# Kernel tuning notes

Hardware: AMD Instinct MI355X
Metric: run time of the kernel (lower is better)

The kernel has to match this reference:

```python
import jax, jax.numpy as jnp
import numpy as np

B, C, H, W = 16, 256, 64, 64
NH, HD = 8, 32  # num_heads, head_dim


def _conv1x1(x, w, b):
    # x: [B,C,H,W], w: [Cout,Cin], b: [Cout] -> [B,Cout,H,W]
    return jnp.einsum('bchw,oc->bohw', x, w) + b[None, :, None, None]


def setup_inputs() -> dict:
    key = jax.random.key(0)
    ks = jax.random.split(key, 11)
    s = 1.0 / np.sqrt(C)
    return {
        'q': jax.random.normal(ks[0], (B, C, H, W), jnp.float32),
        'k': jax.random.normal(ks[1], (B, C, H, W), jnp.float32),
        'v': jax.random.normal(ks[2], (B, C, H, W), jnp.float32),
        'Wq': jax.random.normal(ks[3], (C, C), jnp.float32) * s,
        'bq': jax.random.normal(ks[4], (C,), jnp.float32) * 0.01,
        'Wk': jax.random.normal(ks[5], (C, C), jnp.float32) * s,
        'bk': jax.random.normal(ks[6], (C,), jnp.float32) * 0.01,
        'Wv': jax.random.normal(ks[7], (C, C), jnp.float32) * s,
        'bv': jax.random.normal(ks[8], (C,), jnp.float32) * 0.01,
        'Wo': jax.random.normal(ks[9], (C, C), jnp.float32) * s,
        'bo': jax.random.normal(ks[10], (C,), jnp.float32) * 0.01,
    }


def reference(q, k, v, Wq, bq, Wk, bk, Wv, bv, Wo, bo):
    # 1x1 conv projections, then split heads: [B, NH, HD, H, W]
    qh = _conv1x1(q, Wq, bq).reshape(B, NH, HD, H, W)
    kh = _conv1x1(k, Wk, bk).reshape(B, NH, HD, H, W)
    vh = _conv1x1(v, Wv, bv).reshape(B, NH, HD, H, W)
    # Attention over last two dims: q @ k^T -> [B, NH, HD, H, H], d_k = W
    scale = 1.0 / jnp.sqrt(jnp.float32(W))
    logits = jnp.einsum('bndhw,bndgw->bndhg', qh, kh) * scale
    attn = jax.nn.softmax(logits, axis=-1)  # [B,NH,HD,H,H]
    out = jnp.einsum('bndhg,bndgw->bndhw', attn, vh)  # [B,NH,HD,H,W]
    out = out.reshape(B, C, H, W)  # combine heads
    out = _conv1x1(out, Wo, bo)
    return out, attn
```

## Files before the change

### kernel.cpp

```cpp
#include <hip/hip_runtime.h>

#define NB  16
#define CC  256
#define SH  64
#define SW  64
#define HWP 4096
#define NSLICE (NB * CC)
#define OUT_ELEMS ((size_t)NB * CC * HWP)
#define PADK 40

using bf16x8 = __attribute__((ext_vector_type(8))) short;
using f32x4  = __attribute__((ext_vector_type(4))) float;

__device__ __forceinline__ unsigned pack_hi16(unsigned u0, unsigned u1) {
    return __builtin_amdgcn_perm(u1, u0, 0x07060302u);
}
__device__ __forceinline__ float trunc_bf(unsigned u) {
    union { unsigned u; float f; } v; v.u = u & 0xFFFF0000u; return v.f;
}
__device__ __forceinline__ unsigned fbits(float x) {
    union { float f; unsigned u; } v; v.f = x; return v.u;
}

__global__ __launch_bounds__(256) void proj_mfma_kernel(
    const float* __restrict__ X, const float* __restrict__ W,
    const float* __restrict__ bias, float* __restrict__ Y)
{
    __shared__ short sWhi[128][PADK];
    __shared__ short sWlo[128][PADK];
    __shared__ short sXhi[128][PADK];
    __shared__ short sXlo[128][PADK];

    const int tid = threadIdx.x;
    const int o0  = blockIdx.x * 128;
    const int p0  = blockIdx.y * 128;
    const int b   = blockIdx.z;
    const float* Xb = X + (size_t)b * CC * HWP;

    const int wid  = tid >> 6;
    const int lane = tid & 63;
    const int wr = wid >> 1, wc = wid & 1;
    const int l16 = lane & 15, lq = lane >> 4;

    const int kq = tid & 7;
    const int ooB = tid >> 3;
    const int cb = tid & 7;
    const int pb = tid >> 3;

    f32x4 acc[4][4] = {};

    for (int c0 = 0; c0 < CC; c0 += 32) {
        __syncthreads();

        #pragma unroll
        for (int pass = 0; pass < 4; ++pass) {
            const int oo = ooB + pass * 32;
            const float4 wv = *(const float4*)&W[(size_t)(o0 + oo) * CC + c0 + kq * 4];
            const unsigned u0 = fbits(wv.x), u1 = fbits(wv.y),
                           u2 = fbits(wv.z), u3 = fbits(wv.w);
            const float r0 = wv.x - trunc_bf(u0);
            const float r1 = wv.y - trunc_bf(u1);
            const float r2 = wv.z - trunc_bf(u2);
            const float r3 = wv.w - trunc_bf(u3);
            uint2 hi, lo;
            hi.x = pack_hi16(u0, u1);          hi.y = pack_hi16(u2, u3);
            lo.x = pack_hi16(fbits(r0), fbits(r1));
            lo.y = pack_hi16(fbits(r2), fbits(r3));
            *(uint2*)&sWhi[oo][kq * 4] = hi;
            *(uint2*)&sWlo[oo][kq * 4] = lo;
        }

        {
            const float* xsrc = Xb + (size_t)(c0 + cb * 4) * HWP + p0 + pb * 4;
            const float4 x0 = *(const float4*)(xsrc);
            const float4 x1 = *(const float4*)(xsrc + HWP);
            const float4 x2 = *(const float4*)(xsrc + 2 * HWP);
            const float4 x3 = *(const float4*)(xsrc + 3 * HWP);
            const float c0v[4][4] = {{x0.x, x1.x, x2.x, x3.x},
                                     {x0.y, x1.y, x2.y, x3.y},
                                     {x0.z, x1.z, x2.z, x3.z},
                                     {x0.w, x1.w, x2.w, x3.w}};
            #pragma unroll
            for (int j = 0; j < 4; ++j) {
                const unsigned u0 = fbits(c0v[j][0]), u1 = fbits(c0v[j][1]),
                               u2 = fbits(c0v[j][2]), u3 = fbits(c0v[j][3]);
                const float r0 = c0v[j][0] - trunc_bf(u0);
                const float r1 = c0v[j][1] - trunc_bf(u1);
                const float r2 = c0v[j][2] - trunc_bf(u2);
                const float r3 = c0v[j][3] - trunc_bf(u3);
                uint2 hi, lo;
                hi.x = pack_hi16(u0, u1);          hi.y = pack_hi16(u2, u3);
                lo.x = pack_hi16(fbits(r0), fbits(r1));
                lo.y = pack_hi16(fbits(r2), fbits(r3));
                *(uint2*)&sXhi[pb * 4 + j][cb * 4] = hi;
                *(uint2*)&sXlo[pb * 4 + j][cb * 4] = lo;
            }
        }
        __syncthreads();

        const int aRow = wr * 64 + l16;
        const int bRow = wc * 64 + l16;
        bf16x8 bhi[4], blo[4];
        #pragma unroll
        for (int fn = 0; fn < 4; ++fn) {
            bhi[fn] = *(const bf16x8*)&sXhi[bRow + fn * 16][lq * 8];
            blo[fn] = *(const bf16x8*)&sXlo[bRow + fn * 16][lq * 8];
        }
        #pragma unroll
        for (int fm = 0; fm < 4; ++fm) {
            const bf16x8 ahi = *(const bf16x8*)&sWhi[aRow + fm * 16][lq * 8];
            const bf16x8 alo = *(const bf16x8*)&sWlo[aRow + fm * 16][lq * 8];
            #pragma unroll
            for (int fn = 0; fn < 4; ++fn) {
                acc[fm][fn] = __builtin_amdgcn_mfma_f32_16x16x32_bf16(
                    ahi, bhi[fn], acc[fm][fn], 0, 0, 0);
                acc[fm][fn] = __builtin_amdgcn_mfma_f32_16x16x32_bf16(
                    ahi, blo[fn], acc[fm][fn], 0, 0, 0);
                acc[fm][fn] = __builtin_amdgcn_mfma_f32_16x16x32_bf16(
                    alo, bhi[fn], acc[fm][fn], 0, 0, 0);
            }
        }
    }

    #pragma unroll
    for (int fm = 0; fm < 4; ++fm) {
        #pragma unroll
        for (int j = 0; j < 4; ++j) {
            const int o = o0 + wr * 64 + fm * 16 + lq * 4 + j;
            const float bv = bias[o];
            #pragma unroll
            for (int fn = 0; fn < 4; ++fn) {
                Y[((size_t)b * CC + o) * HWP + p0 + wc * 64 + fn * 16 + l16] =
                    acc[fm][fn][j] + bv;
            }
        }
    }
}

__global__ __launch_bounds__(256) void attn_kernel(
    const float* qh, const float* kh, const float* vh,
    float* attn_out, float* out_pre)
{
    __shared__ float Qt[64][68];
    __shared__ float Kt[64][68];
    __shared__ float Vs[64][68];

    const int tid  = threadIdx.x;
    const int tr   = tid & 15;
    const int tc   = tid >> 4;
    const int s    = blockIdx.x;
    const size_t base = (size_t)s * HWP;

    {
        const int r0 = tc << 2, c0 = tr << 2;
        const float* src = qh + base + r0 * SW + c0;
        const float4 a0 = *(const float4*)(src);
        const float4 a1 = *(const float4*)(src + SW);
        const float4 a2 = *(const float4*)(src + 2 * SW);
        const float4 a3 = *(const float4*)(src + 3 * SW);
        *(float4*)&Qt[c0 + 0][r0] = make_float4(a0.x, a1.x, a2.x, a3.x);
        *(float4*)&Qt[c0 + 1][r0] = make_float4(a0.y, a1.y, a2.y, a3.y);
        *(float4*)&Qt[c0 + 2][r0] = make_float4(a0.z, a1.z, a2.z, a3.z);
        *(float4*)&Qt[c0 + 3][r0] = make_float4(a0.w, a1.w, a2.w, a3.w);
    }
    {
        const int r0 = tc << 2, c0 = tr << 2;
        const float* src = kh + base + r0 * SW + c0;
        const float4 a0 = *(const float4*)(src);
        const float4 a1 = *(const float4*)(src + SW);
        const float4 a2 = *(const float4*)(src + 2 * SW);
        const float4 a3 = *(const float4*)(src + 3 * SW);
        *(float4*)&Kt[c0 + 0][r0] = make_float4(a0.x, a1.x, a2.x, a3.x);
        *(float4*)&Kt[c0 + 1][r0] = make_float4(a0.y, a1.y, a2.y, a3.y);
        *(float4*)&Kt[c0 + 2][r0] = make_float4(a0.z, a1.z, a2.z, a3.z);
        *(float4*)&Kt[c0 + 3][r0] = make_float4(a0.w, a1.w, a2.w, a3.w);
    }
    #pragma unroll
    for (int it = 0; it < 4; ++it) {
        const int g = tc + it * 16;
        const float4 vv = *(const float4*)&vh[base + g * SW + (tr << 2)];
        *(float4*)&Vs[g][tr << 2] = vv;
    }
    __syncthreads();

    float accq[4][4] = {};
    #pragma unroll
    for (int w = 0; w < 64; ++w) {
        const float4 av = *(const float4*)&Qt[w][tc << 2];
        const float4 bv = *(const float4*)&Kt[w][tr << 2];
        const float a[4] = {av.x, av.y, av.z, av.w};
        const float g[4] = {bv.x, bv.y, bv.z, bv.w};
        #pragma unroll
        for (int i = 0; i < 4; ++i)
            #pragma unroll
            for (int j = 0; j < 4; ++j)
                accq[i][j] = fmaf(a[i], g[j], accq[i][j]);
    }

    float p[4][4];
    #pragma unroll
    for (int i = 0; i < 4; ++i) {
        float l0 = accq[i][0] * 0.125f;
        float l1 = accq[i][1] * 0.125f;
        float l2 = accq[i][2] * 0.125f;
        float l3 = accq[i][3] * 0.125f;
        float m = fmaxf(fmaxf(l0, l1), fmaxf(l2, l3));
        m = fmaxf(m, __shfl_xor(m, 1));
        m = fmaxf(m, __shfl_xor(m, 2));
        m = fmaxf(m, __shfl_xor(m, 4));
        m = fmaxf(m, __shfl_xor(m, 8));
        const float e0 = __expf(l0 - m);
        const float e1 = __expf(l1 - m);
        const float e2 = __expf(l2 - m);
        const float e3 = __expf(l3 - m);
        float sum = e0 + e1 + e2 + e3;
        sum += __shfl_xor(sum, 1);
        sum += __shfl_xor(sum, 2);
        sum += __shfl_xor(sum, 4);
        sum += __shfl_xor(sum, 8);
        const float rs = 1.0f / sum;
        p[i][0] = e0 * rs; p[i][1] = e1 * rs;
        p[i][2] = e2 * rs; p[i][3] = e3 * rs;
    }

    #pragma unroll
    for (int i = 0; i < 4; ++i) {
        float4 r = make_float4(p[i][0], p[i][1], p[i][2], p[i][3]);
        *(float4*)&attn_out[base + (size_t)((tc << 2) + i) * SH + (tr << 2)] = r;
    }

    __syncthreads();
    #pragma unroll
    for (int j = 0; j < 4; ++j) {
        *(float4*)&Qt[(tr << 2) + j][tc << 2] =
            make_float4(p[0][j], p[1][j], p[2][j], p[3][j]);
    }
    __syncthreads();

    float o[4][4] = {};
    #pragma unroll
    for (int g = 0; g < 64; ++g) {
        const float4 av = *(const float4*)&Qt[g][tc << 2];
        const float4 bv = *(const float4*)&Vs[g][tr << 2];
        const float a[4] = {av.x, av.y, av.z, av.w};
        const float v[4] = {bv.x, bv.y, bv.z, bv.w};
        #pragma unroll
        for (int i = 0; i < 4; ++i)
            #pragma unroll
            for (int j = 0; j < 4; ++j)
                o[i][j] = fmaf(a[i], v[j], o[i][j]);
    }
    #pragma unroll
    for (int i = 0; i < 4; ++i) {
        float4 r = make_float4(o[i][0], o[i][1], o[i][2], o[i][3]);
        *(float4*)&out_pre[base + (size_t)((tc << 2) + i) * SW + (tr << 2)] = r;
    }
}

extern "C" void kernel_launch(void* const* d_in, const int* in_sizes, int n_in,
                              void* d_out, int out_size, void* d_ws, size_t ws_size,
                              hipStream_t stream) {
    (void)in_sizes; (void)n_in; (void)out_size; (void)ws_size;

    const float* q  = (const float*)d_in[0];
    const float* k  = (const float*)d_in[1];
    const float* v  = (const float*)d_in[2];
    const float* Wq = (const float*)d_in[3];
    const float* bq = (const float*)d_in[4];
    const float* Wk = (const float*)d_in[5];
    const float* bk = (const float*)d_in[6];
    const float* Wv = (const float*)d_in[7];
    const float* bv = (const float*)d_in[8];
    const float* Wo = (const float*)d_in[9];
    const float* bo = (const float*)d_in[10];

    float* out  = (float*)d_out;
    float* attn = out + OUT_ELEMS;

    float* vh      = out;
    float* kh      = attn;
    float* qh      = (float*)d_ws;
    float* out_pre = qh;

    const dim3 gproj(2, 32, NB);
    const dim3 blk(256);

    proj_mfma_kernel<<<gproj, blk, 0, stream>>>(q, Wq, bq, qh);
    proj_mfma_kernel<<<gproj, blk, 0, stream>>>(k, Wk, bk, kh);
    proj_mfma_kernel<<<gproj, blk, 0, stream>>>(v, Wv, bv, vh);

    attn_kernel<<<dim3(NSLICE), blk, 0, stream>>>(qh, kh, vh, attn, out_pre);

    proj_mfma_kernel<<<gproj, blk, 0, stream>>>(out_pre, Wo, bo, out);
}
```

Before: 463.3 us.

## Use split-bf16 MFMA for attention and merge QKV projections into one launch

Rewrites the per-slice attention kernel so each wavefront handles one 64x64 slice. Both matmuls (QK^T and PV) run on bf16 MFMA with a hi/lo three-product split to keep near-fp32 accuracy, replacing scalar fp32 FMAs and the block-wide LDS transposes. The three Q/K/V projections become one launch with a 48-deep z grid to cut launch overhead and improve GPU fill. The costs are strided global loads for V, narrower attn/out stores, and more register pressure from holding K and V fragments.

```diff
diff --git a/kernel.cpp b/kernel.cpp
--- a/kernel.cpp
+++ b/kernel.cpp
@@ -12,19 +12,35 @@
 using bf16x8 = __attribute__((ext_vector_type(8))) short;
 using f32x4  = __attribute__((ext_vector_type(4))) float;
 
-__device__ __forceinline__ unsigned pack_hi16(unsigned u0, unsigned u1) {
+static __device__ __forceinline__ unsigned pack_hi16(unsigned u0, unsigned u1) {
     return __builtin_amdgcn_perm(u1, u0, 0x07060302u);
 }
-__device__ __forceinline__ float trunc_bf(unsigned u) {
+static __device__ __forceinline__ float trunc_bf(unsigned u) {
     union { unsigned u; float f; } v; v.u = u & 0xFFFF0000u; return v.f;
 }
-__device__ __forceinline__ unsigned fbits(float x) {
+static __device__ __forceinline__ unsigned fbits(float x) {
     union { float f; unsigned u; } v; v.f = x; return v.u;
 }
 
-__global__ __launch_bounds__(256) void proj_mfma_kernel(
+static __device__ __forceinline__ void split8(float4 a, float4 b,
+                                              bf16x8& hi, bf16x8& lo) {
+    union { bf16x8 v; unsigned u[4]; } H, L;
+    const float f[8] = {a.x, a.y, a.z, a.w, b.x, b.y, b.z, b.w};
+    #pragma unroll
+    for (int j = 0; j < 4; ++j) {
+        const unsigned u0 = fbits(f[2 * j]), u1 = fbits(f[2 * j + 1]);
+        const float r0 = f[2 * j]     - trunc_bf(u0);
+        const float r1 = f[2 * j + 1] - trunc_bf(u1);
+        H.u[j] = pack_hi16(u0, u1);
+        L.u[j] = pack_hi16(fbits(r0), fbits(r1));
+    }
+    hi = H.v; lo = L.v;
+}
+
+static __device__ __forceinline__ void proj_body(
     const float* __restrict__ X, const float* __restrict__ W,
-    const float* __restrict__ bias, float* __restrict__ Y)
+    const float* __restrict__ bias, float* __restrict__ Y,
+    int b, int o0, int p0)
 {
     __shared__ short sWhi[128][PADK];
     __shared__ short sWlo[128][PADK];
@@ -32,9 +48,6 @@
     __shared__ short sXlo[128][PADK];
 
     const int tid = threadIdx.x;
-    const int o0  = blockIdx.x * 128;
-    const int p0  = blockIdx.y * 128;
-    const int b   = blockIdx.z;
     const float* Xb = X + (size_t)b * CC * HWP;
 
     const int wid  = tid >> 6;
@@ -51,7 +64,6 @@
 
     for (int c0 = 0; c0 < CC; c0 += 32) {
         __syncthreads();
-
         #pragma unroll
         for (int pass = 0; pass < 4; ++pass) {
             const int oo = ooB + pass * 32;
@@ -69,7 +81,6 @@
             *(uint2*)&sWhi[oo][kq * 4] = hi;
             *(uint2*)&sWlo[oo][kq * 4] = lo;
         }
-
         {
             const float* xsrc = Xb + (size_t)(c0 + cb * 4) * HWP + p0 + pb * 4;
             const float4 x0 = *(const float4*)(xsrc);
@@ -137,123 +148,155 @@
     }
 }
 
-__global__ __launch_bounds__(256) void attn_kernel(
+__global__ __launch_bounds__(256) void proj_qkv_kernel(
+    const float* __restrict__ q, const float* __restrict__ Wq,
+    const float* __restrict__ bq, float* __restrict__ qh,
+    const float* __restrict__ k, const float* __restrict__ Wk,
+    const float* __restrict__ bk, float* __restrict__ kh,
+    const float* __restrict__ v, const float* __restrict__ Wv,
+    const float* __restrict__ bv, float* __restrict__ vh)
+{
+    const int which = blockIdx.z >> 4;
+    const int b     = blockIdx.z & 15;
+    const float* X  = (which == 0) ? q  : (which == 1) ? k  : v;
+    const float* W  = (which == 0) ? Wq : (which == 1) ? Wk : Wv;
+    const float* bi = (which == 0) ? bq : (which == 1) ? bk : bv;
+    float*       Y  = (which == 0) ? qh : (which == 1) ? kh : vh;
+    proj_body(X, W, bi, Y, b, blockIdx.x * 128, blockIdx.y * 128);
+}
+
+__global__ __launch_bounds__(256) void proj_o_kernel(
+    const float* __restrict__ X, const float* __restrict__ W,
+    const float* __restrict__ bias, float* __restrict__ Y)
+{
+    proj_body(X, W, bias, Y, blockIdx.z, blockIdx.x * 128, blockIdx.y * 128);
+}
+
+__global__ __launch_bounds__(256) void attn_mfma_kernel(
     const float* qh, const float* kh, const float* vh,
     float* attn_out, float* out_pre)
 {
-    __shared__ float Qt[64][68];
-    __shared__ float Kt[64][68];
-    __shared__ float Vs[64][68];
+    __shared__ float Pb[4][16][68];
 
     const int tid  = threadIdx.x;
-    const int tr   = tid & 15;
-    const int tc   = tid >> 4;
-    const int s    = blockIdx.x;
+    const int wid  = tid >> 6;
+    const int lane = tid & 63;
+    const int l16  = lane & 15;
+    const int lq   = lane >> 4;
+
+    const int s = blockIdx.x * 4 + wid;
     const size_t base = (size_t)s * HWP;
-
-    {
-        const int r0 = tc << 2, c0 = tr << 2;
-        const float* src = qh + base + r0 * SW + c0;
-        const float4 a0 = *(const float4*)(src);
-        const float4 a1 = *(const float4*)(src + SW);
-        const float4 a2 = *(const float4*)(src + 2 * SW);
-        const float4 a3 = *(const float4*)(src + 3 * SW);
-        *(float4*)&Qt[c0 + 0][r0] = make_float4(a0.x, a1.x, a2.x, a3.x);
-        *(float4*)&Qt[c0 + 1][r0] = make_float4(a0.y, a1.y, a2.y, a3.y);
-        *(float4*)&Qt[c0 + 2][r0] = make_float4(a0.z, a1.z, a2.z, a3.z);
-        *(float4*)&Qt[c0 + 3][r0] = make_float4(a0.w, a1.w, a2.w, a3.w);
-    }
-    {
-        const int r0 = tc << 2, c0 = tr << 2;
-        const float* src = kh + base + r0 * SW + c0;
-        const float4 a0 = *(const float4*)(src);
-        const float4 a1 = *(const float4*)(src + SW);
-        const float4 a2 = *(const float4*)(src + 2 * SW);
-        const float4 a3 = *(const float4*)(src + 3 * SW);
-        *(float4*)&Kt[c0 + 0][r0] = make_float4(a0.x, a1.x, a2.x, a3.x);
-        *(float4*)&Kt[c0 + 1][r0] = make_float4(a0.y, a1.y, a2.y, a3.y);
-        *(float4*)&Kt[c0 + 2][r0] = make_float4(a0.z, a1.z, a2.z, a3.z);
-        *(float4*)&Kt[c0 + 3][r0] = make_float4(a0.w, a1.w, a2.w, a3.w);
-    }
-    #pragma unroll
-    for (int it = 0; it < 4; ++it) {
-        const int g = tc + it * 16;
-        const float4 vv = *(const float4*)&vh[base + g * SW + (tr << 2)];
-        *(float4*)&Vs[g][tr << 2] = vv;
-    }
-    __syncthreads();
-
-    float accq[4][4] = {};
-    #pragma unroll
-    for (int w = 0; w < 64; ++w) {
-        const float4 av = *(const float4*)&Qt[w][tc << 2];
-        const float4 bv = *(const float4*)&Kt[w][tr << 2];
-        const float a[4] = {av.x, av.y, av.z, av.w};
-        const float g[4] = {bv.x, bv.y, bv.z, bv.w};
-        #pragma unroll
-        for (int i = 0; i < 4; ++i)
-            #pragma unroll
-            for (int j = 0; j < 4; ++j)
-                accq[i][j] = fmaf(a[i], g[j], accq[i][j]);
-    }
-
-    float p[4][4];
-    #pragma unroll
-    for (int i = 0; i < 4; ++i) {
-        float l0 = accq[i][0] * 0.125f;
-        float l1 = accq[i][1] * 0.125f;
-        float l2 = accq[i][2] * 0.125f;
-        float l3 = accq[i][3] * 0.125f;
-        float m = fmaxf(fmaxf(l0, l1), fmaxf(l2, l3));
-        m = fmaxf(m, __shfl_xor(m, 1));
-        m = fmaxf(m, __shfl_xor(m, 2));
-        m = fmaxf(m, __shfl_xor(m, 4));
-        m = fmaxf(m, __shfl_xor(m, 8));
-        const float e0 = __expf(l0 - m);
-        const float e1 = __expf(l1 - m);
-        const float e2 = __expf(l2 - m);
-        const float e3 = __expf(l3 - m);
-        float sum = e0 + e1 + e2 + e3;
-        sum += __shfl_xor(sum, 1);
-        sum += __shfl_xor(sum, 2);
-        sum += __shfl_xor(sum, 4);
-        sum += __shfl_xor(sum, 8);
-        const float rs = 1.0f / sum;
-        p[i][0] = e0 * rs; p[i][1] = e1 * rs;
-        p[i][2] = e2 * rs; p[i][3] = e3 * rs;
-    }
-
-    #pragma unroll
-    for (int i = 0; i < 4; ++i) {
-        float4 r = make_float4(p[i][0], p[i][1], p[i][2], p[i][3]);
-        *(float4*)&attn_out[base + (size_t)((tc << 2) + i) * SH + (tr << 2)] = r;
-    }
-
-    __syncthreads();
-    #pragma unroll
-    for (int j = 0; j < 4; ++j) {
-        *(float4*)&Qt[(tr << 2) + j][tc << 2] =
-            make_float4(p[0][j], p[1][j], p[2][j], p[3][j]);
-    }
-    __syncthreads();
-
-    float o[4][4] = {};
-    #pragma unroll
-    for (int g = 0; g < 64; ++g) {
-        const float4 av = *(const float4*)&Qt[g][tc << 2];
-        const float4 bv = *(const float4*)&Vs[g][tr << 2];
-        const float a[4] = {av.x, av.y, av.z, av.w};
-        const float v[4] = {bv.x, bv.y, bv.z, bv.w};
-        #pragma unroll
-        for (int i = 0; i < 4; ++i)
-            #pragma unroll
-            for (int j = 0; j < 4; ++j)
-                o[i][j] = fmaf(a[i], v[j], o[i][j]);
-    }
-    #pragma unroll
-    for (int i = 0; i < 4; ++i) {
-        float4 r = make_float4(o[i][0], o[i][1], o[i][2], o[i][3]);
-        *(float4*)&out_pre[base + (size_t)((tc << 2) + i) * SW + (tr << 2)] = r;
+    const float* Q = qh + base;
+    const float* K = kh + base;
+    const float* V = vh + base;
+    float (*P)[68] = Pb[wid];
+
+    bf16x8 Khi[4][2], Klo[4][2];
+    #pragma unroll
+    for (int nt = 0; nt < 4; ++nt)
+        #pragma unroll
+        for (int ks = 0; ks < 2; ++ks) {
+            const float* src = K + (nt * 16 + l16) * SW + ks * 32 + lq * 8;
+            split8(*(const float4*)src, *(const float4*)(src + 4),
+                   Khi[nt][ks], Klo[nt][ks]);
+        }
+
+    f32x4 acc[4][4] = {};
+    #pragma unroll
+    for (int mt = 0; mt < 4; ++mt) {
+        bf16x8 Qhi[2], Qlo[2];
+        #pragma unroll
+        for (int ks = 0; ks < 2; ++ks) {
+            const float* src = Q + (mt * 16 + l16) * SW + ks * 32 + lq * 8;
+            split8(*(const float4*)src, *(const float4*)(src + 4),
+                   Qhi[ks], Qlo[ks]);
+        }
+        #pragma unroll
+        for (int nt = 0; nt < 4; ++nt)
+            #pragma unroll
+            for (int ks = 0; ks < 2; ++ks) {
+                acc[mt][nt] = __builtin_amdgcn_mfma_f32_16x16x32_bf16(
+                    Qhi[ks], Khi[nt][ks], acc[mt][nt], 0, 0, 0);
+                acc[mt][nt] = __builtin_amdgcn_mfma_f32_16x16x32_bf16(
+                    Qhi[ks], Klo[nt][ks], acc[mt][nt], 0, 0, 0);
+                acc[mt][nt] = __builtin_amdgcn_mfma_f32_16x16x32_bf16(
+                    Qlo[ks], Khi[nt][ks], acc[mt][nt], 0, 0, 0);
+            }
+    }
+
+    bf16x8 Vhi[4][2], Vlo[4][2];
+    #pragma unroll
+    for (int nt = 0; nt < 4; ++nt)
+        #pragma unroll
+        for (int ks = 0; ks < 2; ++ks) {
+            const float* vcol = V + nt * 16 + l16;
+            float f[8];
+            #pragma unroll
+            for (int e = 0; e < 8; ++e)
+                f[e] = vcol[(ks * 32 + lq * 8 + e) * SW];
+            split8(make_float4(f[0], f[1], f[2], f[3]),
+                   make_float4(f[4], f[5], f[6], f[7]),
+                   Vhi[nt][ks], Vlo[nt][ks]);
+        }
+
+    #pragma unroll
+    for (int mt = 0; mt < 4; ++mt) {
+        #pragma unroll
+        for (int r = 0; r < 4; ++r) {
+            float l0 = acc[mt][0][r] * 0.125f;
+            float l1 = acc[mt][1][r] * 0.125f;
+            float l2 = acc[mt][2][r] * 0.125f;
+            float l3 = acc[mt][3][r] * 0.125f;
+            float m = fmaxf(fmaxf(l0, l1), fmaxf(l2, l3));
+            m = fmaxf(m, __shfl_xor(m, 1));
+            m = fmaxf(m, __shfl_xor(m, 2));
+            m = fmaxf(m, __shfl_xor(m, 4));
+            m = fmaxf(m, __shfl_xor(m, 8));
+            const float e0 = __expf(l0 - m);
+            const float e1 = __expf(l1 - m);
+            const float e2 = __expf(l2 - m);
+            const float e3 = __expf(l3 - m);
+            float sum = e0 + e1 + e2 + e3;
+            sum += __shfl_xor(sum, 1);
+            sum += __shfl_xor(sum, 2);
+            sum += __shfl_xor(sum, 4);
+            sum += __shfl_xor(sum, 8);
+            const float rs = 1.0f / sum;
+            const float p0 = e0 * rs, p1 = e1 * rs, p2 = e2 * rs, p3 = e3 * rs;
+            const int h = mt * 16 + lq * 4 + r;
+            float* gdst = attn_out + base + (size_t)h * SH;
+            gdst[0 * 16 + l16] = p0;
+            gdst[1 * 16 + l16] = p1;
+            gdst[2 * 16 + l16] = p2;
+            gdst[3 * 16 + l16] = p3;
+            const int hr = lq * 4 + r;
+            P[hr][0 * 16 + l16] = p0;
+            P[hr][1 * 16 + l16] = p1;
+            P[hr][2 * 16 + l16] = p2;
+            P[hr][3 * 16 + l16] = p3;
+        }
+        f32x4 o[4] = {};
+        #pragma unroll
+        for (int ks = 0; ks < 2; ++ks) {
+            const float* src = &P[l16][ks * 32 + lq * 8];
+            bf16x8 Phi, Plo;
+            split8(*(const float4*)src, *(const float4*)(src + 4), Phi, Plo);
+            #pragma unroll
+            for (int nt = 0; nt < 4; ++nt) {
+                o[nt] = __builtin_amdgcn_mfma_f32_16x16x32_bf16(
+                    Phi, Vhi[nt][ks], o[nt], 0, 0, 0);
+                o[nt] = __builtin_amdgcn_mfma_f32_16x16x32_bf16(
+                    Phi, Vlo[nt][ks], o[nt], 0, 0, 0);
+                o[nt] = __builtin_amdgcn_mfma_f32_16x16x32_bf16(
+                    Plo, Vhi[nt][ks], o[nt], 0, 0, 0);
+            }
+        }
+        #pragma unroll
+        for (int nt = 0; nt < 4; ++nt)
+            #pragma unroll
+            for (int r = 0; r < 4; ++r)
+                out_pre[base + (size_t)(mt * 16 + lq * 4 + r) * SW + nt * 16 + l16] =
+                    o[nt][r];
     }
 }
 
@@ -282,14 +325,13 @@
     float* qh      = (float*)d_ws;
     float* out_pre = qh;
 
-    const dim3 gproj(2, 32, NB);
     const dim3 blk(256);
 
-    proj_mfma_kernel<<<gproj, blk, 0, stream>>>(q, Wq, bq, qh);
-    proj_mfma_kernel<<<gproj, blk, 0, stream>>>(k, Wk, bk, kh);
-    proj_mfma_kernel<<<gproj, blk, 0, stream>>>(v, Wv, bv, vh);
-
-    attn_kernel<<<dim3(NSLICE), blk, 0, stream>>>(qh, kh, vh, attn, out_pre);
-
-    proj_mfma_kernel<<<gproj, blk, 0, stream>>>(out_pre, Wo, bo, out);
-}
+    proj_qkv_kernel<<<dim3(2, 32, 48), blk, 0, stream>>>(
+        q, Wq, bq, qh, k, Wk, bk, kh, v, Wv, bv, vh);
+
+    attn_mfma_kernel<<<dim3(NSLICE / 4), blk, 0, stream>>>(
+        qh, kh, vh, attn, out_pre);
+
+    proj_o_kernel<<<dim3(2, 32, 16), blk, 0, stream>>>(out_pre, Wo, bo, out);
+}
```

New measurement: 454.8 us. No clear change (-1.8%).
